# Optimization experiments

Hardware: AMD Instinct MI355X
Metric: run time of the kernel (lower is better)

The kernel has to match this reference:

```python
import jax, jax.numpy as jnp
import numpy as np

N = 100000      # nodes
E = 1600000     # edges (before self-loops)
F_IN = 128      # num_features
C = 32          # embedding_dim / output_dim per head
H = 4           # heads
SLOPE = 0.2     # PyG GATv2Conv default negative_slope


def setup_inputs() -> dict:
    key = jax.random.key(0)
    ks = jax.random.split(key, 16)
    def w(k, shp, fan):
        return jax.random.normal(k, shp, jnp.float32) / np.float32(np.sqrt(fan))
    return {
        "x": jax.random.normal(ks[0], (N, F_IN), jnp.float32),
        "edge_index": jax.random.randint(ks[1], (2, E), 0, N, jnp.int32),
        "W1l": w(ks[2], (F_IN, H * C), F_IN),
        "W1r": w(ks[3], (F_IN, H * C), F_IN),
        "att1": w(ks[4], (H, C), C),
        "b1": jnp.zeros((H * C,), jnp.float32),
        "W2l": w(ks[5], (H * C, H * C), H * C),
        "W2r": w(ks[6], (H * C, H * C), H * C),
        "att2": w(ks[7], (H, C), C),
        "b2": jnp.zeros((H * C,), jnp.float32),
        "W3l": w(ks[8], (H * C, H * C), H * C),
        "W3r": w(ks[9], (H * C, H * C), H * C),
        "att3": w(ks[10], (H, C), C),
        "b3": jnp.zeros((C,), jnp.float32),
    }


def gatv2_conv(x, src, dst, Wl, Wr, att, b, concat):
    """GATv2Conv: gather -> LeakyReLU attention -> segment softmax -> scatter-add."""
    n = x.shape[0]
    h, c = att.shape
    xl = (x @ Wl).reshape(n, h, c)   # source-side projection
    xr = (x @ Wr).reshape(n, h, c)   # target-side projection
    e = jax.nn.leaky_relu(xl[src] + xr[dst], SLOPE)          # [E, H, C]
    logits = jnp.einsum('ehc,hc->eh', e, att)                # [E, H]
    m = jax.ops.segment_max(logits, dst, num_segments=n)     # per-dst max
    ex = jnp.exp(logits - m[dst])
    den = jax.ops.segment_sum(ex, dst, num_segments=n)
    alpha = ex / den[dst]                                    # [E, H]
    out = jax.ops.segment_sum(alpha[:, :, None] * xl[src], dst, num_segments=n)  # [N,H,C]
    out = out.reshape(n, h * c) if concat else out.mean(axis=1)
    return out + b


def reference(x, edge_index, W1l, W1r, att1, b1, W2l, W2r, att2, b2, W3l, W3r, att3, b3):
    n = x.shape[0]
    loops = jnp.arange(n, dtype=edge_index.dtype)            # PyG adds self-loops
    src = jnp.concatenate([edge_index[0], loops])
    dst = jnp.concatenate([edge_index[1], loops])
    h = jax.nn.relu(gatv2_conv(x, src, dst, W1l, W1r, att1, b1, True))
    h = jax.nn.relu(gatv2_conv(h, src, dst, W2l, W2r, att2, b2, True))
    h = jax.nn.relu(gatv2_conv(h, src, dst, W3l, W3r, att3, b3, False))
    return h
```

## Files before the change

### kernel.cpp

```cpp
#include <hip/hip_runtime.h>
#include <hip/hip_bf16.h>
#include <hip/hip_fp16.h>

#define SLOPE 0.2f

typedef __attribute__((ext_vector_type(8))) short bf16x8;
typedef __attribute__((ext_vector_type(4))) float f32x4;

__device__ __forceinline__ unsigned short bf16_rn(float f) {
    unsigned u = __float_as_uint(f);
    return (unsigned short)((u + 0x7FFFu + ((u >> 16) & 1u)) >> 16);
}
__device__ __forceinline__ float bf16_to_f32(unsigned short s) {
    return __uint_as_float(((unsigned)s) << 16);
}


__global__ __launch_bounds__(256) void fat_prep(const float* __restrict__ W0, const float* __restrict__ W1,
                                                const float* __restrict__ W2, const float* __restrict__ W3,
                                                const float* __restrict__ W4, const float* __restrict__ W5,
                                                unsigned short* __restrict__ Wtab,
                                                const int* __restrict__ dstv, int* __restrict__ deg, int E) {
    int b = blockIdx.x, t = threadIdx.x;
    if (b < 384) {
        int j = b >> 6;
        int e = ((b & 63) << 8) + t;
        const float* W = (j == 0) ? W0 : (j == 1) ? W1 : (j == 2) ? W2
                       : (j == 3) ? W3 : (j == 4) ? W4 : W5;
        int L = j >> 1, side = j & 1;
        unsigned short* hiT = Wtab + (size_t)L * 65536 + side * 16384;
        unsigned short* loT = hiT + 32768;
        int n = e >> 7, k = e & 127;
        float x = W[k * 128 + n];
        unsigned short h = bf16_rn(x);
        hiT[e] = h;
        loT[e] = bf16_rn(x - bf16_to_f32(h));
    } else {
        int i = (b - 384) * 256 + t;
        if (i < E) atomicAdd(&deg[dstv[i]], 1);
    }
}


__global__ __launch_bounds__(256) void k_scan(const int* __restrict__ in, int* __restrict__ out,
                                              int* bsums, int n) {
    __shared__ int wsum[4];
    int t = threadIdx.x;
    int base = blockIdx.x * 1024 + t * 4;
    int v0 = (base + 0 < n) ? in[base + 0] : 0;
    int v1 = (base + 1 < n) ? in[base + 1] : 0;
    int v2 = (base + 2 < n) ? in[base + 2] : 0;
    int v3 = (base + 3 < n) ? in[base + 3] : 0;
    int tsum = v0 + v1 + v2 + v3;
    int lane = t & 63, wid = t >> 6;
    int x = tsum;
    #pragma unroll
    for (int d = 1; d < 64; d <<= 1) {
        int y = __shfl_up(x, d);
        if (lane >= d) x += y;
    }
    if (lane == 63) wsum[wid] = x;
    __syncthreads();
    if (t == 0) {
        int a = 0;
        for (int w = 0; w < 4; ++w) { int b = wsum[w]; wsum[w] = a; a += b; }
    }
    __syncthreads();
    int excl = x - tsum + wsum[wid];
    if (base + 0 < n) out[base + 0] = excl;
    if (base + 1 < n) out[base + 1] = excl + v0;
    if (base + 2 < n) out[base + 2] = excl + v0 + v1;
    if (base + 3 < n) out[base + 3] = excl + v0 + v1 + v2;
    if (bsums != nullptr && t == 255) bsums[blockIdx.x] = excl + tsum;
}

__global__ __launch_bounds__(256) void k_scan_add(const int* __restrict__ dscan,
                                                  const int* __restrict__ boff,
                                                  int* __restrict__ rowptr, int* __restrict__ bcur,
                                                  int n, int total) {
    int i = blockIdx.x * 256 + threadIdx.x;
    if (i < n) {
        int v = dscan[i] + boff[i >> 10];
        rowptr[i] = v;
        if ((i & 255) == 0) bcur[i >> 8] = v;
    }
    if (i == n) rowptr[n] = total;
}


__global__ __launch_bounds__(256) void k_binA(const int* __restrict__ srcv, const int* __restrict__ dstv,
                                              int* __restrict__ bcur, int2* __restrict__ edge2,
                                              int E, int NB) {
    __shared__ int lcnt[512];
    __shared__ int lbase[512];
    int t = threadIdx.x;
    int base = blockIdx.x * 16384;
    for (int b = t; b < 512; b += 256) lcnt[b] = 0;
    __syncthreads();
    #pragma unroll 4
    for (int j = 0; j < 64; ++j) {
        int idx = base + j * 256 + t;
        if (idx < E) atomicAdd(&lcnt[dstv[idx] >> 8], 1);
    }
    __syncthreads();
    for (int b = t; b < NB; b += 256) {
        int c = lcnt[b];
        lbase[b] = c ? atomicAdd(&bcur[b], c) : 0;
        lcnt[b] = 0;
    }
    __syncthreads();
    #pragma unroll 4
    for (int j = 0; j < 64; ++j) {
        int idx = base + j * 256 + t;
        if (idx < E) {
            int s = srcv[idx], d = dstv[idx];
            int bk = d >> 8;
            int off = atomicAdd(&lcnt[bk], 1);
            edge2[lbase[bk] + off] = make_int2(s, d);
        }
    }
}


__global__ __launch_bounds__(256) void k_binB(const int* __restrict__ rowptr,
                                              const int2* __restrict__ edge2,
                                              int* __restrict__ col, int N) {
    __shared__ int cur[256];
    int t = threadIdx.x;
    int dstbase = blockIdx.x << 8;
    int dd = dstbase + t;
    cur[t] = (dd < N) ? rowptr[dd] : 0;
    __syncthreads();
    int beg = rowptr[dstbase];
    int hi = dstbase + 256; if (hi > N) hi = N;
    int endd = rowptr[hi];
    for (int e = beg + t; e < endd; e += 256) {
        int2 ed = edge2[e];
        int pos = atomicAdd(&cur[ed.y & 255], 1);
        col[pos] = ed.x;
    }
}


#define LDS_A_HI 0
#define LDS_A_LO 10240
#define LDS_B_HI 20480
#define LDS_B_LO 30720

__device__ __forceinline__ void gemm_block(const float* __restrict__ X,
                                           const unsigned short* __restrict__ WL,
                                           __half* __restrict__ Y0, float* __restrict__ Y1,
                                           int M, int tile, int ysel,
                                           unsigned char* lds, int t) {
    const unsigned short* whi = WL + ysel * 16384;
    const unsigned short* wlo = whi + 32768;
    int row0 = tile * 128;
    int lane = t & 63, w = t >> 6;
    int ml = lane & 15, q = lane >> 4;
    int sm = t >> 1, sh = t & 1;
    int srow = row0 + sm;
    bool svalid = srow < M;

    f32x4 acc[2][8];
    #pragma unroll
    for (int i = 0; i < 2; ++i)
        #pragma unroll
        for (int j = 0; j < 8; ++j) acc[i][j] = (f32x4){0.f, 0.f, 0.f, 0.f};

    for (int ks = 0; ks < 4; ++ks) {
        int k0 = ks * 32;
        {
            float v[16];
            if (svalid) {
                const float* src = X + (size_t)srow * 128 + k0 + sh * 16;
                *(float4*)&v[0]  = *(const float4*)&src[0];
                *(float4*)&v[4]  = *(const float4*)&src[4];
                *(float4*)&v[8]  = *(const float4*)&src[8];
                *(float4*)&v[12] = *(const float4*)&src[12];
            } else {
                #pragma unroll
                for (int j = 0; j < 16; ++j) v[j] = 0.f;
            }
            unsigned hw[8], lw[8];
            #pragma unroll
            for (int j = 0; j < 8; ++j) {
                unsigned short h0 = bf16_rn(v[2 * j]);
                unsigned short h1 = bf16_rn(v[2 * j + 1]);
                unsigned short l0 = bf16_rn(v[2 * j] - bf16_to_f32(h0));
                unsigned short l1 = bf16_rn(v[2 * j + 1] - bf16_to_f32(h1));
                hw[j] = (unsigned)h0 | ((unsigned)h1 << 16);
                lw[j] = (unsigned)l0 | ((unsigned)l1 << 16);
            }
            unsigned char* pa = lds + LDS_A_HI + sm * 80 + sh * 32;
            *(uint4*)(pa)      = *(uint4*)&hw[0];
            *(uint4*)(pa + 16) = *(uint4*)&hw[4];
            unsigned char* pl = lds + LDS_A_LO + sm * 80 + sh * 32;
            *(uint4*)(pl)      = *(uint4*)&lw[0];
            *(uint4*)(pl + 16) = *(uint4*)&lw[4];
        }
        {
            #pragma unroll
            for (int cc = 0; cc < 2; ++cc) {
                int c = t + cc * 256;
                int n = c >> 2, kc = (c & 3) * 8;
                *(uint4*)(lds + LDS_B_HI + n * 80 + (c & 3) * 16) =
                    *(const uint4*)(whi + n * 128 + k0 + kc);
                *(uint4*)(lds + LDS_B_LO + n * 80 + (c & 3) * 16) =
                    *(const uint4*)(wlo + n * 128 + k0 + kc);
            }
        }
        __syncthreads();
        bf16x8 ah[2], al[2];
        #pragma unroll
        for (int mt = 0; mt < 2; ++mt) {
            int am = w * 32 + mt * 16 + ml;
            ah[mt] = *(const bf16x8*)(lds + LDS_A_HI + am * 80 + q * 16);
            al[mt] = *(const bf16x8*)(lds + LDS_A_LO + am * 80 + q * 16);
        }
        #pragma unroll
        for (int nt = 0; nt < 8; ++nt) {
            int bn = nt * 16 + ml;
            bf16x8 bh = *(const bf16x8*)(lds + LDS_B_HI + bn * 80 + q * 16);
            bf16x8 bl = *(const bf16x8*)(lds + LDS_B_LO + bn * 80 + q * 16);
            #pragma unroll
            for (int mt = 0; mt < 2; ++mt) {
                acc[mt][nt] = __builtin_amdgcn_mfma_f32_16x16x32_bf16(ah[mt], bh, acc[mt][nt], 0, 0, 0);
                acc[mt][nt] = __builtin_amdgcn_mfma_f32_16x16x32_bf16(ah[mt], bl, acc[mt][nt], 0, 0, 0);
                acc[mt][nt] = __builtin_amdgcn_mfma_f32_16x16x32_bf16(al[mt], bh, acc[mt][nt], 0, 0, 0);
            }
        }
        __syncthreads();
    }

    if (ysel == 0) {
        #pragma unroll
        for (int mt = 0; mt < 2; ++mt) {
            int rbase = row0 + w * 32 + mt * 16 + q * 4;
            #pragma unroll
            for (int r = 0; r < 4; ++r) {
                int row = rbase + r;
                if (row < M) {
                    #pragma unroll
                    for (int nt = 0; nt < 8; ++nt)
                        Y0[(size_t)row * 128 + nt * 16 + ml] = __float2half(acc[mt][nt][r]);
                }
            }
        }
    } else {
        #pragma unroll
        for (int mt = 0; mt < 2; ++mt) {
            int rbase = row0 + w * 32 + mt * 16 + q * 4;
            #pragma unroll
            for (int r = 0; r < 4; ++r) {
                int row = rbase + r;
                if (row < M) {
                    #pragma unroll
                    for (int nt = 0; nt < 8; ++nt)
                        Y1[(size_t)row * 128 + nt * 16 + ml] = acc[mt][nt][r];
                }
            }
        }
    }
}

__global__ __launch_bounds__(256) void k_gemm(const float* __restrict__ X,
                                              const unsigned short* __restrict__ WL,
                                              __half* __restrict__ Y0, float* __restrict__ Y1, int M) {
    __shared__ __align__(16) unsigned char lds[40960];
    gemm_block(X, WL, Y0, Y1, M, blockIdx.x, blockIdx.y, lds, threadIdx.x);
}


__device__ __forceinline__ float quadsum(float t) {
    t += __int_as_float(__builtin_amdgcn_update_dpp(0, __float_as_int(t), 0xB1, 0xf, 0xf, true));
    t += __int_as_float(__builtin_amdgcn_update_dpp(0, __float_as_int(t), 0x4E, 0xf, 0xf, true));
    return t;
}

template <bool MEAN>
__global__ __launch_bounds__(256) void fused_gat(const __half* __restrict__ XLh,
                                                 const float* __restrict__ XR,
                                                 const float* __restrict__ att,
                                                 const float* __restrict__ bias,
                                                 const int* __restrict__ rowptr,
                                                 const int* __restrict__ col,
                                                 float* __restrict__ OUT, int N) {
    int wave = (blockIdx.x * blockDim.x + threadIdx.x) >> 6;
    int lane = threadIdx.x & 63;
    int g = lane >> 4, sub = lane & 15;
    int dst = wave * 4 + g;
    bool vd = dst < N;
    int d0 = vd ? dst : 0;

    int start = vd ? rowptr[d0] : 0;
    int end   = vd ? rowptr[d0 + 1] : 0;

    float xr[8], av[8];
    {
        const float* xrp = &XR[(size_t)d0 * 128 + sub * 8];
        *(float4*)&xr[0] = *(const float4*)&xrp[0];
        *(float4*)&xr[4] = *(const float4*)&xrp[4];
        *(float4*)&av[0] = *(const float4*)&att[sub * 8];
        *(float4*)&av[4] = *(const float4*)&att[sub * 8 + 4];
    }

    int deg = end - start;
    int md = max(deg, __shfl_xor(deg, 16));
    md = max(md, __shfl_xor(md, 32));

    float acc[8];
    float s;
    {
        uint4 r = *(const uint4*)&XLh[(size_t)d0 * 128 + sub * 8];
        float xs[8];
        const __half2* h = (const __half2*)&r;
        #pragma unroll
        for (int qq = 0; qq < 4; ++qq) {
            float2 f = __half22float2(h[qq]);
            xs[2 * qq] = f.x; xs[2 * qq + 1] = f.y;
        }
        float dS = 0.f;
        #pragma unroll
        for (int j = 0; j < 8; ++j) {
            float u = xs[j] + xr[j];
            u = fmaxf(u, SLOPE * u);
            dS = fmaf(u, av[j], dS);
        }
        float tS = quadsum(dS);
        float wS = __expf(fminf(tS, 80.f));
        s = wS;
        #pragma unroll
        for (int j = 0; j < 8; ++j) acc[j] = wS * xs[j];
    }

    for (int i = 0; i < md; i += 2) {
        int pA = start + i, pB = start + i + 1;
        bool vA = pA < end, vB = pB < end;
        int iA = col[vA ? pA : 0];
        int iB = col[vB ? pB : 0];
        uint4 rA = *(const uint4*)&XLh[(size_t)iA * 128 + sub * 8];
        uint4 rB = *(const uint4*)&XLh[(size_t)iB * 128 + sub * 8];
        float xA[8], xB[8];
        {
            const __half2* hA = (const __half2*)&rA;
            const __half2* hB = (const __half2*)&rB;
            #pragma unroll
            for (int qq = 0; qq < 4; ++qq) {
                float2 fA = __half22float2(hA[qq]);
                float2 fB = __half22float2(hB[qq]);
                xA[2 * qq] = fA.x; xA[2 * qq + 1] = fA.y;
                xB[2 * qq] = fB.x; xB[2 * qq + 1] = fB.y;
            }
        }
        float dA = 0.f, dB = 0.f;
        #pragma unroll
        for (int j = 0; j < 8; ++j) {
            float uA = xA[j] + xr[j];
            float uB = xB[j] + xr[j];
            uA = fmaxf(uA, SLOPE * uA);
            uB = fmaxf(uB, SLOPE * uB);
            dA = fmaf(uA, av[j], dA);
            dB = fmaf(uB, av[j], dB);
        }
        float tA = quadsum(dA);
        float tB = quadsum(dB);
        float wA = __expf(fminf(tA, 80.f));
        float wB = __expf(fminf(tB, 80.f));
        wA = vA ? wA : 0.f;
        wB = vB ? wB : 0.f;
        s += wA + wB;
        #pragma unroll
        for (int j = 0; j < 8; ++j) {
            acc[j] = fmaf(wA, xA[j], acc[j]);
            acc[j] = fmaf(wB, xB[j], acc[j]);
        }
    }

    float rs = 1.0f / s;
    if (MEAN) {
        float o[8];
        #pragma unroll
        for (int j = 0; j < 8; ++j) {
            float v = acc[j] * rs;
            v += __shfl_xor(v, 4);
            v += __shfl_xor(v, 8);
            o[j] = fmaxf(fmaf(v, 0.25f, bias[sub * 8 + j]), 0.f);
        }
        if (vd && sub < 4) {
            *(float4*)&OUT[(size_t)dst * 32 + sub * 8]     = *(float4*)&o[0];
            *(float4*)&OUT[(size_t)dst * 32 + sub * 8 + 4] = *(float4*)&o[4];
        }
    } else {
        float o[8];
        #pragma unroll
        for (int j = 0; j < 8; ++j)
            o[j] = fmaxf(fmaf(acc[j], rs, bias[sub * 8 + j]), 0.f);
        if (vd) {
            *(float4*)&OUT[(size_t)dst * 128 + sub * 8]     = *(float4*)&o[0];
            *(float4*)&OUT[(size_t)dst * 128 + sub * 8 + 4] = *(float4*)&o[4];
        }
    }
}


extern "C" void kernel_launch(void* const* d_in, const int* in_sizes, int n_in,
                              void* d_out, int out_size, void* d_ws, size_t ws_size,
                              hipStream_t stream) {
    const float* x   = (const float*)d_in[0];
    const int*   ei  = (const int*)d_in[1];
    const float* W1l = (const float*)d_in[2];
    const float* W1r = (const float*)d_in[3];
    const float* at1 = (const float*)d_in[4];
    const float* b1  = (const float*)d_in[5];
    const float* W2l = (const float*)d_in[6];
    const float* W2r = (const float*)d_in[7];
    const float* at2 = (const float*)d_in[8];
    const float* b2  = (const float*)d_in[9];
    const float* W3l = (const float*)d_in[10];
    const float* W3r = (const float*)d_in[11];
    const float* at3 = (const float*)d_in[12];
    const float* b3  = (const float*)d_in[13];
    float* out = (float*)d_out;

    int N = in_sizes[0] / 128;
    int E = in_sizes[1] / 2;
    const int* srcv = ei;
    const int* dstv = ei + E;
    int NB = (N + 255) >> 8;

    char* p = (char*)d_ws;
    auto alloc = [&](size_t bytes) -> void* {
        void* r = (void*)p;
        p += (bytes + 255) & ~(size_t)255;
        return r;
    };
    __half* XLh = (__half*)alloc((size_t)N * 128 * 2);
    float*  XR  = (float*)alloc((size_t)N * 128 * 4);
    float*  H   = (float*)alloc((size_t)N * 128 * 4);
    int* rowptr = (int*)alloc((size_t)(N + 1) * 4);
    int* deg    = (int*)alloc((size_t)N * 4);
    int* dscan  = (int*)alloc((size_t)N * 4);
    int* bcur   = (int*)alloc((size_t)NB * 4);
    int* bsum   = (int*)alloc(1024 * 4);
    int* boff   = (int*)alloc(1024 * 4);
    int* col    = (int*)alloc((size_t)E * 4);
    int2* edge2 = (int2*)alloc((size_t)E * 8);
    unsigned short* Wtab = (unsigned short*)alloc((size_t)6 * 65536 * 2);

    int tiles = (N + 127) / 128;
    int nfb = (N + 15) / 16;
    int eb = (E + 255) / 256;

    hipMemsetAsync(deg, 0, (size_t)N * 4, stream);
    fat_prep<<<384 + eb, 256, 0, stream>>>(W1l, W1r, W2l, W2r, W3l, W3r, Wtab, dstv, deg, E);
    int nb = (N + 1023) / 1024;
    k_scan<<<nb, 256, 0, stream>>>(deg, dscan, bsum, N);
    k_scan<<<1, 256, 0, stream>>>(bsum, boff, nullptr, nb);
    k_scan_add<<<(N + 256) / 256, 256, 0, stream>>>(dscan, boff, rowptr, bcur, N, E);
    k_binA<<<(E + 16383) / 16384, 256, 0, stream>>>(srcv, dstv, bcur, edge2, E, NB);
    k_binB<<<NB, 256, 0, stream>>>(rowptr, edge2, col, N);
    k_gemm<<<dim3(tiles, 2), 256, 0, stream>>>(x, Wtab, XLh, XR, N);
    fused_gat<false><<<nfb, 256, 0, stream>>>(XLh, XR, at1, b1, rowptr, col, H, N);
    k_gemm<<<dim3(tiles, 2), 256, 0, stream>>>(H, Wtab + 1 * 65536, XLh, XR, N);
    fused_gat<false><<<nfb, 256, 0, stream>>>(XLh, XR, at2, b2, rowptr, col, H, N);
    k_gemm<<<dim3(tiles, 2), 256, 0, stream>>>(H, Wtab + 2 * 65536, XLh, XR, N);
    fused_gat<true><<<nfb, 256, 0, stream>>>(XLh, XR, at3, b3, rowptr, col, out, N);
}
```

Measured before the change: 590.3 us.

## Sort destination nodes by degree for balanced waves and pack math into float2

Adds a degree histogram, scan and fill pass that builds a permutation of nodes ordered by in-degree, capped at 63. The fused GAT kernels then assign each wave four nodes of similar degree, so the per-wave loop bound set by the largest degree wastes fewer iterations. Separately, the per-lane math is rewritten with two-wide float vectors so the compiler can emit packed FP32 instructions. The cost is three extra small kernels, a memset, and scattered, non-coalesced reads of XR and writes of the output in permuted order.

```diff
diff --git a/kernel.cpp b/kernel.cpp
--- a/kernel.cpp
+++ b/kernel.cpp
@@ -6,6 +6,7 @@
 
 typedef __attribute__((ext_vector_type(8))) short bf16x8;
 typedef __attribute__((ext_vector_type(4))) float f32x4;
+typedef __attribute__((ext_vector_type(2))) float f32x2;
 
 __device__ __forceinline__ unsigned short bf16_rn(float f) {
     unsigned u = __float_as_uint(f);
@@ -88,6 +89,62 @@
 }
 
 
+__global__ __launch_bounds__(256) void k_dhist(const int* __restrict__ deg, int* __restrict__ ghist, int N) {
+    __shared__ int h[64];
+    int t = threadIdx.x;
+    if (t < 64) h[t] = 0;
+    __syncthreads();
+    #pragma unroll
+    for (int j = 0; j < 4; ++j) {
+        int i = blockIdx.x * 1024 + j * 256 + t;
+        if (i < N) atomicAdd(&h[min(deg[i], 63)], 1);
+    }
+    __syncthreads();
+    if (t < 64 && h[t]) atomicAdd(&ghist[t], h[t]);
+}
+
+__global__ __launch_bounds__(64) void k_dscan(const int* __restrict__ ghist, int* __restrict__ dcur) {
+    int t = threadIdx.x;
+    int v = ghist[t];
+    int x = v;
+    #pragma unroll
+    for (int d = 1; d < 64; d <<= 1) {
+        int y = __shfl_up(x, d);
+        if (t >= d) x += y;
+    }
+    dcur[t] = x - v;
+}
+
+__global__ __launch_bounds__(256) void k_dfill(const int* __restrict__ deg, int* __restrict__ dcur,
+                                               int* __restrict__ ord, int N) {
+    __shared__ int lcnt[64], lbase[64];
+    int t = threadIdx.x;
+    if (t < 64) lcnt[t] = 0;
+    __syncthreads();
+    #pragma unroll
+    for (int j = 0; j < 4; ++j) {
+        int i = blockIdx.x * 1024 + j * 256 + t;
+        if (i < N) atomicAdd(&lcnt[min(deg[i], 63)], 1);
+    }
+    __syncthreads();
+    if (t < 64) {
+        int c = lcnt[t];
+        lbase[t] = c ? atomicAdd(&dcur[t], c) : 0;
+        lcnt[t] = 0;
+    }
+    __syncthreads();
+    #pragma unroll
+    for (int j = 0; j < 4; ++j) {
+        int i = blockIdx.x * 1024 + j * 256 + t;
+        if (i < N) {
+            int b = min(deg[i], 63);
+            int off = atomicAdd(&lcnt[b], 1);
+            ord[lbase[b] + off] = i;
+        }
+    }
+}
+
+
 __global__ __launch_bounds__(256) void k_binA(const int* __restrict__ srcv, const int* __restrict__ dstv,
                                               int* __restrict__ bcur, int2* __restrict__ edge2,
                                               int E, int NB) {
@@ -120,7 +177,6 @@
         }
     }
 }
-
 
 __global__ __launch_bounds__(256) void k_binB(const int* __restrict__ rowptr,
                                               const int2* __restrict__ edge2,
@@ -277,6 +333,16 @@
     return t;
 }
 
+__device__ __forceinline__ void cvt8(const uint4& r, f32x2* x) {
+    union { uint4 u; __half2 h[4]; } cv;
+    cv.u = r;
+    #pragma unroll
+    for (int q = 0; q < 4; ++q) {
+        float2 f = __half22float2(cv.h[q]);
+        x[q] = (f32x2){f.x, f.y};
+    }
+}
+
 template <bool MEAN>
 __global__ __launch_bounds__(256) void fused_gat(const __half* __restrict__ XLh,
                                                  const float* __restrict__ XR,
@@ -284,53 +350,57 @@
                                                  const float* __restrict__ bias,
                                                  const int* __restrict__ rowptr,
                                                  const int* __restrict__ col,
+                                                 const int* __restrict__ ord,
                                                  float* __restrict__ OUT, int N) {
     int wave = (blockIdx.x * blockDim.x + threadIdx.x) >> 6;
     int lane = threadIdx.x & 63;
     int g = lane >> 4, sub = lane & 15;
-    int dst = wave * 4 + g;
-    bool vd = dst < N;
-    int d0 = vd ? dst : 0;
+    int idx = wave * 4 + g;
+    bool vd = idx < N;
+    int d0 = vd ? ord[idx] : 0;
 
     int start = vd ? rowptr[d0] : 0;
     int end   = vd ? rowptr[d0 + 1] : 0;
 
-    float xr[8], av[8];
+    f32x2 xr2[4], av2[4];
     {
+        float xr[8], av[8];
         const float* xrp = &XR[(size_t)d0 * 128 + sub * 8];
         *(float4*)&xr[0] = *(const float4*)&xrp[0];
         *(float4*)&xr[4] = *(const float4*)&xrp[4];
         *(float4*)&av[0] = *(const float4*)&att[sub * 8];
         *(float4*)&av[4] = *(const float4*)&att[sub * 8 + 4];
+        #pragma unroll
+        for (int q = 0; q < 4; ++q) {
+            xr2[q] = (f32x2){xr[2 * q], xr[2 * q + 1]};
+            av2[q] = (f32x2){av[2 * q], av[2 * q + 1]};
+        }
     }
 
     int deg = end - start;
     int md = max(deg, __shfl_xor(deg, 16));
     md = max(md, __shfl_xor(md, 32));
 
-    float acc[8];
+    f32x2 acc2[4];
     float s;
     {
         uint4 r = *(const uint4*)&XLh[(size_t)d0 * 128 + sub * 8];
-        float xs[8];
-        const __half2* h = (const __half2*)&r;
-        #pragma unroll
-        for (int qq = 0; qq < 4; ++qq) {
-            float2 f = __half22float2(h[qq]);
-            xs[2 * qq] = f.x; xs[2 * qq + 1] = f.y;
-        }
-        float dS = 0.f;
-        #pragma unroll
-        for (int j = 0; j < 8; ++j) {
-            float u = xs[j] + xr[j];
-            u = fmaxf(u, SLOPE * u);
-            dS = fmaf(u, av[j], dS);
-        }
-        float tS = quadsum(dS);
+        f32x2 xs[4];
+        cvt8(r, xs);
+        f32x2 d2 = (f32x2){0.f, 0.f};
+        #pragma unroll
+        for (int q = 0; q < 4; ++q) {
+            f32x2 u = xs[q] + xr2[q];
+            f32x2 lu = u * SLOPE;
+            u.x = fmaxf(u.x, lu.x);
+            u.y = fmaxf(u.y, lu.y);
+            d2 += u * av2[q];
+        }
+        float tS = quadsum(d2.x + d2.y);
         float wS = __expf(fminf(tS, 80.f));
         s = wS;
         #pragma unroll
-        for (int j = 0; j < 8; ++j) acc[j] = wS * xs[j];
+        for (int q = 0; q < 4; ++q) acc2[q] = xs[q] * wS;
     }
 
     for (int i = 0; i < md; i += 2) {
@@ -340,39 +410,32 @@
         int iB = col[vB ? pB : 0];
         uint4 rA = *(const uint4*)&XLh[(size_t)iA * 128 + sub * 8];
         uint4 rB = *(const uint4*)&XLh[(size_t)iB * 128 + sub * 8];
-        float xA[8], xB[8];
-        {
-            const __half2* hA = (const __half2*)&rA;
-            const __half2* hB = (const __half2*)&rB;
-            #pragma unroll
-            for (int qq = 0; qq < 4; ++qq) {
-                float2 fA = __half22float2(hA[qq]);
-                float2 fB = __half22float2(hB[qq]);
-                xA[2 * qq] = fA.x; xA[2 * qq + 1] = fA.y;
-                xB[2 * qq] = fB.x; xB[2 * qq + 1] = fB.y;
-            }
-        }
-        float dA = 0.f, dB = 0.f;
-        #pragma unroll
-        for (int j = 0; j < 8; ++j) {
-            float uA = xA[j] + xr[j];
-            float uB = xB[j] + xr[j];
-            uA = fmaxf(uA, SLOPE * uA);
-            uB = fmaxf(uB, SLOPE * uB);
-            dA = fmaf(uA, av[j], dA);
-            dB = fmaf(uB, av[j], dB);
-        }
-        float tA = quadsum(dA);
-        float tB = quadsum(dB);
+        f32x2 xA[4], xB[4];
+        cvt8(rA, xA);
+        cvt8(rB, xB);
+        f32x2 dA2 = (f32x2){0.f, 0.f}, dB2 = (f32x2){0.f, 0.f};
+        #pragma unroll
+        for (int q = 0; q < 4; ++q) {
+            f32x2 uA = xA[q] + xr2[q];
+            f32x2 uB = xB[q] + xr2[q];
+            f32x2 lA = uA * SLOPE;
+            f32x2 lB = uB * SLOPE;
+            uA.x = fmaxf(uA.x, lA.x); uA.y = fmaxf(uA.y, lA.y);
+            uB.x = fmaxf(uB.x, lB.x); uB.y = fmaxf(uB.y, lB.y);
+            dA2 += uA * av2[q];
+            dB2 += uB * av2[q];
+        }
+        float tA = quadsum(dA2.x + dA2.y);
+        float tB = quadsum(dB2.x + dB2.y);
         float wA = __expf(fminf(tA, 80.f));
         float wB = __expf(fminf(tB, 80.f));
         wA = vA ? wA : 0.f;
         wB = vB ? wB : 0.f;
         s += wA + wB;
         #pragma unroll
-        for (int j = 0; j < 8; ++j) {
-            acc[j] = fmaf(wA, xA[j], acc[j]);
-            acc[j] = fmaf(wB, xB[j], acc[j]);
+        for (int q = 0; q < 4; ++q) {
+            acc2[q] += xA[q] * wA;
+            acc2[q] += xB[q] * wB;
         }
     }
 
@@ -380,24 +443,27 @@
     if (MEAN) {
         float o[8];
         #pragma unroll
-        for (int j = 0; j < 8; ++j) {
-            float v = acc[j] * rs;
-            v += __shfl_xor(v, 4);
-            v += __shfl_xor(v, 8);
-            o[j] = fmaxf(fmaf(v, 0.25f, bias[sub * 8 + j]), 0.f);
+        for (int q = 0; q < 4; ++q) {
+            float vx = acc2[q].x * rs, vy = acc2[q].y * rs;
+            vx += __shfl_xor(vx, 4); vy += __shfl_xor(vy, 4);
+            vx += __shfl_xor(vx, 8); vy += __shfl_xor(vy, 8);
+            o[2 * q]     = fmaxf(fmaf(vx, 0.25f, bias[sub * 8 + 2 * q]), 0.f);
+            o[2 * q + 1] = fmaxf(fmaf(vy, 0.25f, bias[sub * 8 + 2 * q + 1]), 0.f);
         }
         if (vd && sub < 4) {
-            *(float4*)&OUT[(size_t)dst * 32 + sub * 8]     = *(float4*)&o[0];
-            *(float4*)&OUT[(size_t)dst * 32 + sub * 8 + 4] = *(float4*)&o[4];
+            *(float4*)&OUT[(size_t)d0 * 32 + sub * 8]     = *(float4*)&o[0];
+            *(float4*)&OUT[(size_t)d0 * 32 + sub * 8 + 4] = *(float4*)&o[4];
         }
     } else {
         float o[8];
         #pragma unroll
-        for (int j = 0; j < 8; ++j)
-            o[j] = fmaxf(fmaf(acc[j], rs, bias[sub * 8 + j]), 0.f);
+        for (int q = 0; q < 4; ++q) {
+            o[2 * q]     = fmaxf(fmaf(acc2[q].x, rs, bias[sub * 8 + 2 * q]), 0.f);
+            o[2 * q + 1] = fmaxf(fmaf(acc2[q].y, rs, bias[sub * 8 + 2 * q + 1]), 0.f);
+        }
         if (vd) {
-            *(float4*)&OUT[(size_t)dst * 128 + sub * 8]     = *(float4*)&o[0];
-            *(float4*)&OUT[(size_t)dst * 128 + sub * 8 + 4] = *(float4*)&o[4];
+            *(float4*)&OUT[(size_t)d0 * 128 + sub * 8]     = *(float4*)&o[0];
+            *(float4*)&OUT[(size_t)d0 * 128 + sub * 8 + 4] = *(float4*)&o[4];
         }
     }
 }
@@ -440,9 +506,12 @@
     int* rowptr = (int*)alloc((size_t)(N + 1) * 4);
     int* deg    = (int*)alloc((size_t)N * 4);
     int* dscan  = (int*)alloc((size_t)N * 4);
+    int* ord    = (int*)alloc((size_t)N * 4);
     int* bcur   = (int*)alloc((size_t)NB * 4);
     int* bsum   = (int*)alloc(1024 * 4);
     int* boff   = (int*)alloc(1024 * 4);
+    int* ghist  = (int*)alloc(64 * 4);
+    int* dcur   = (int*)alloc(64 * 4);
     int* col    = (int*)alloc((size_t)E * 4);
     int2* edge2 = (int2*)alloc((size_t)E * 8);
     unsigned short* Wtab = (unsigned short*)alloc((size_t)6 * 65536 * 2);
@@ -450,19 +519,24 @@
     int tiles = (N + 127) / 128;
     int nfb = (N + 15) / 16;
     int eb = (E + 255) / 256;
+    int db = (N + 1023) / 1024;
 
     hipMemsetAsync(deg, 0, (size_t)N * 4, stream);
+    hipMemsetAsync(ghist, 0, 64 * 4, stream);
     fat_prep<<<384 + eb, 256, 0, stream>>>(W1l, W1r, W2l, W2r, W3l, W3r, Wtab, dstv, deg, E);
     int nb = (N + 1023) / 1024;
     k_scan<<<nb, 256, 0, stream>>>(deg, dscan, bsum, N);
     k_scan<<<1, 256, 0, stream>>>(bsum, boff, nullptr, nb);
     k_scan_add<<<(N + 256) / 256, 256, 0, stream>>>(dscan, boff, rowptr, bcur, N, E);
+    k_dhist<<<db, 256, 0, stream>>>(deg, ghist, N);
+    k_dscan<<<1, 64, 0, stream>>>(ghist, dcur);
+    k_dfill<<<db, 256, 0, stream>>>(deg, dcur, ord, N);
     k_binA<<<(E + 16383) / 16384, 256, 0, stream>>>(srcv, dstv, bcur, edge2, E, NB);
     k_binB<<<NB, 256, 0, stream>>>(rowptr, edge2, col, N);
     k_gemm<<<dim3(tiles, 2), 256, 0, stream>>>(x, Wtab, XLh, XR, N);
-    fused_gat<false><<<nfb, 256, 0, stream>>>(XLh, XR, at1, b1, rowptr, col, H, N);
+    fused_gat<false><<<nfb, 256, 0, stream>>>(XLh, XR, at1, b1, rowptr, col, ord, H, N);
     k_gemm<<<dim3(tiles, 2), 256, 0, stream>>>(H, Wtab + 1 * 65536, XLh, XR, N);
-    fused_gat<false><<<nfb, 256, 0, stream>>>(XLh, XR, at2, b2, rowptr, col, H, N);
+    fused_gat<false><<<nfb, 256, 0, stream>>>(XLh, XR, at2, b2, rowptr, col, ord, H, N);
     k_gemm<<<dim3(tiles, 2), 256, 0, stream>>>(H, Wtab + 2 * 65536, XLh, XR, N);
-    fused_gat<true><<<nfb, 256, 0, stream>>>(XLh, XR, at3, b3, rowptr, col, out, N);
-}
+    fused_gat<true><<<nfb, 256, 0, stream>>>(XLh, XR, at3, b3, rowptr, col, ord, out, N);
+}
```

Measured after the change: 597.5 us. Within noise of the previous version (+1.2%).
